# Kernel optimization log

Measured on AMD Instinct MI355X. Metric: run time of the kernel, lower is better.

Reference implementation:

```python
import jax, jax.numpy as jnp
import numpy as np

N_NODES = 100000
N_EDGES = 1600000
F_IN = 128      # dataset.num_features
HID = 128       # hidden_dim (heads=1)
HID_POST = 128  # hidden_dim_post
EDGE_DIM = 16
N_CLASSES = 16
NEG_SLOPE = 0.2  # PyG GATConv default leaky_relu slope


def setup_inputs() -> dict:
    key = jax.random.key(0)
    ks = jax.random.split(key, 16)
    s = 0.1  # weight scale
    inp = {
        "x": jax.random.normal(ks[0], (N_NODES, F_IN), jnp.float32),
        "edge_attr": jax.random.normal(ks[1], (N_EDGES, EDGE_DIM), jnp.float32),
        "W0": jax.random.normal(ks[2], (F_IN, HID), jnp.float32) * s,
        "a_src0": jax.random.normal(ks[3], (HID,), jnp.float32) * s,
        "a_dst0": jax.random.normal(ks[4], (HID,), jnp.float32) * s,
        "We0": jax.random.normal(ks[5], (EDGE_DIM, HID), jnp.float32) * s,
        "a_e0": jax.random.normal(ks[6], (HID,), jnp.float32) * s,
        "b0": jnp.zeros((HID,), jnp.float32),
        "W1": jax.random.normal(ks[7], (HID, HID), jnp.float32) * s,
        "a_src1": jax.random.normal(ks[8], (HID,), jnp.float32) * s,
        "a_dst1": jax.random.normal(ks[9], (HID,), jnp.float32) * s,
        "We1": jax.random.normal(ks[10], (EDGE_DIM, HID), jnp.float32) * s,
        "a_e1": jax.random.normal(ks[11], (HID,), jnp.float32) * s,
        "b1": jnp.zeros((HID,), jnp.float32),
        "lin1_w": jax.random.normal(ks[12], (HID, HID_POST), jnp.float32) * s,
        "lin1_b": jnp.zeros((HID_POST,), jnp.float32),
        "lin2_w": jax.random.normal(ks[13], (HID_POST, N_CLASSES), jnp.float32) * s,
        "lin2_b": jnp.zeros((N_CLASSES,), jnp.float32),
        "edge_index": jax.random.randint(ks[14], (2, N_EDGES), 0, N_NODES, jnp.int64),
    }
    return inp


def gat_conv(x, src, dst, edge_attr, W, a_s, a_d, We, a_e, b):
    """PyG GATConv, heads=1, edge_dim set, add_self_loops=True (fill_value='mean')."""
    n = x.shape[0]
    xl = x @ W                       # [N, HID] shared lin for src/dst
    alpha_src_n = xl @ a_s           # [N]
    alpha_dst_n = xl @ a_d           # [N]
    # self loops: edge_attr filled with per-target-node mean of incoming edge_attr
    deg = jax.ops.segment_sum(jnp.ones(src.shape[0], x.dtype), dst, num_segments=n)
    ea_mean = jax.ops.segment_sum(edge_attr, dst, num_segments=n) / jnp.maximum(deg, 1.0)[:, None]
    loop = jnp.arange(n, dtype=src.dtype)
    src_f = jnp.concatenate([src, loop])
    dst_f = jnp.concatenate([dst, loop])
    ea_f = jnp.concatenate([edge_attr, ea_mean], axis=0)  # [E+N, EDGE_DIM]
    alpha_edge = (ea_f @ We) @ a_e                        # [E+N]
    alpha = jax.nn.leaky_relu(
        alpha_src_n[src_f] + alpha_dst_n[dst_f] + alpha_edge, NEG_SLOPE
    )
    # segment softmax over destination node (every node has its self loop -> nonempty)
    amax = jax.ops.segment_max(alpha, dst_f, num_segments=n)
    ex = jnp.exp(alpha - amax[dst_f])
    denom = jax.ops.segment_sum(ex, dst_f, num_segments=n)
    w = ex / denom[dst_f]                                 # [E+N]
    out = jax.ops.segment_sum(xl[src_f] * w[:, None], dst_f, num_segments=n)
    return out + b


def reference(x, edge_attr, W0, a_src0, a_dst0, We0, a_e0, b0,
              W1, a_src1, a_dst1, We1, a_e1, b1,
              lin1_w, lin1_b, lin2_w, lin2_b, edge_index):
    src, dst = edge_index[0], edge_index[1]
    # dropout layers are identity in eval mode
    h = jax.nn.relu(gat_conv(x, src, dst, edge_attr, W0, a_src0, a_dst0, We0, a_e0, b0))
    h = jax.nn.relu(gat_conv(h, src, dst, edge_attr, W1, a_src1, a_dst1, We1, a_e1, b1))
    h = jax.nn.relu(h @ lin1_w + lin1_b)
    logits = h @ lin2_w + lin2_b
    return jax.nn.log_softmax(logits, axis=-1)
```

## Files before the change

### kernel.cpp

```cpp
#include <hip/hip_runtime.h>
#include <math.h>

#define N_NODES 100000
#define N_EDGES 1600000
#define NEG 0.2f
#define MAXDEG 128
#define WPB 4

__device__ __forceinline__ float lrelu(float x){ return x > 0.f ? x : NEG*x; }
__device__ __forceinline__ unsigned short f2bf(float f){
  unsigned int u = __float_as_uint(f);
  u += 0x7FFFu + ((u >> 16) & 1u);
  return (unsigned short)(u >> 16);
}
__device__ __forceinline__ unsigned xcc_id(){
  unsigned x;
  asm volatile("s_getreg_b32 %0, hwreg(HW_REG_XCC_ID)" : "=s"(x));
  return x & 7u;
}

__global__ __launch_bounds__(256) void k_deg(const int* __restrict__ dst, const float* __restrict__ eatt,
    const float* __restrict__ We0, const float* __restrict__ ae0,
    const float* __restrict__ We1, const float* __restrict__ ae1,
    int* __restrict__ deg8, int* __restrict__ rank, float2* __restrict__ ae01){
  __shared__ float wea[32];
  int t = threadIdx.x;
  if (t < 32){
    const float* W = (t < 16) ? We0 : We1;
    const float* a = (t < 16) ? ae0 : ae1;
    int r = t & 15;
    float acc = 0.f;
    #pragma unroll
    for (int j=0;j<128;j++) acc += W[r*128+j]*a[j];
    wea[t] = acc;
  }
  __syncthreads();
  unsigned xcc = xcc_id();
  int* mydeg = deg8 + (size_t)xcc * N_NODES;
  int e = blockIdx.x*256 + t;
  if (e >= N_EDGES) return;
  const float4* p = (const float4*)(eatt + (size_t)e*16);
  float4 a0=p[0], a1=p[1], a2=p[2], a3=p[3];
  float f0 = a0.x*wea[0] +a0.y*wea[1] +a0.z*wea[2] +a0.w*wea[3]
           + a1.x*wea[4] +a1.y*wea[5] +a1.z*wea[6] +a1.w*wea[7]
           + a2.x*wea[8] +a2.y*wea[9] +a2.z*wea[10]+a2.w*wea[11]
           + a3.x*wea[12]+a3.y*wea[13]+a3.z*wea[14]+a3.w*wea[15];
  float f1 = a0.x*wea[16]+a0.y*wea[17]+a0.z*wea[18]+a0.w*wea[19]
           + a1.x*wea[20]+a1.y*wea[21]+a1.z*wea[22]+a1.w*wea[23]
           + a2.x*wea[24]+a2.y*wea[25]+a2.z*wea[26]+a2.w*wea[27]
           + a3.x*wea[28]+a3.y*wea[29]+a3.z*wea[30]+a3.w*wea[31];
  int r = atomicAdd(&mydeg[dst[e]], 1);
  rank[e] = r | (int)(xcc << 24);
  ae01[e] = make_float2(f0, f1);
}

__global__ __launch_bounds__(256) void k_scan_a(const int* __restrict__ deg8, int* __restrict__ deg,
    int* __restrict__ incl, int* __restrict__ bsum){
  __shared__ int s[256];
  int t = threadIdx.x; int i = blockIdx.x*256 + t;
  int v = 0;
  if (i < N_NODES){
    #pragma unroll
    for (int x=0;x<8;x++) v += deg8[(size_t)x*N_NODES + i];
    deg[i] = v;
  }
  s[t] = v; __syncthreads();
  for (int off=1; off<256; off<<=1){
    int u = (t>=off)? s[t-off] : 0; __syncthreads();
    s[t] += u; __syncthreads();
  }
  if (i < N_NODES) incl[i] = s[t];
  if (t == 255) bsum[blockIdx.x] = s[t];
}
__global__ __launch_bounds__(512) void k_scan_b(const int* __restrict__ bsum, int* __restrict__ bexcl, int nb){
  __shared__ int s[512];
  int t = threadIdx.x;
  int v = (t<nb)? bsum[t] : 0;
  s[t] = v; __syncthreads();
  for (int off=1; off<512; off<<=1){
    int u = (t>=off)? s[t-off] : 0; __syncthreads();
    s[t] += u; __syncthreads();
  }
  if (t<nb) bexcl[t] = s[t]-v;
}
__global__ __launch_bounds__(256) void k_scan_c(const int* __restrict__ incl, const int* __restrict__ deg,
    const int* __restrict__ bexcl, const int* __restrict__ deg8,
    int* __restrict__ rowptr, int* __restrict__ rowptr8){
  int i = blockIdx.x*256+threadIdx.x;
  if (i < N_NODES){
    int base = incl[i] - deg[i] + bexcl[blockIdx.x];
    rowptr[i] = base;
    int run = base;
    #pragma unroll
    for (int x=0;x<8;x++){
      rowptr8[(size_t)i*8 + x] = run;
      run += deg8[(size_t)x*N_NODES + i];
    }
  }
  if (i == 0) rowptr[N_NODES] = N_EDGES;
}

__global__ __launch_bounds__(256) void k_fillf(const int* __restrict__ src, const int* __restrict__ dst,
     const int* __restrict__ rank, const float2* __restrict__ ae01,
     const int* __restrict__ rowptr8, uint4* __restrict__ csr){
  int e = blockIdx.x*256+threadIdx.x;
  if (e >= N_EDGES) return;
  int d = dst[e];
  unsigned rk = (unsigned)rank[e];
  float2 ae = ae01[e];
  int pos = rowptr8[(size_t)d*8 + (rk >> 24)] + (int)(rk & 0xFFFFFFu);
  csr[pos] = make_uint4((unsigned)src[e], __float_as_uint(ae.x), __float_as_uint(ae.y), 0u);
}

__global__ __launch_bounds__(256) void k_gemm(const float* __restrict__ X, const float* __restrict__ W,
    const float* __restrict__ bias, float* __restrict__ Y, unsigned short* __restrict__ Ybf,
    const float* __restrict__ a_s, const float* __restrict__ a_d,
    float* __restrict__ asrc, float* __restrict__ adst, int M, int relu){
  __shared__ float Xs[16][68];
  __shared__ float Ws[16][128];
  __shared__ float as_s[128], ad_s[128];
  int t = threadIdx.x;
  if (a_s && t < 128){ as_s[t] = a_s[t]; ad_s[t] = a_d[t]; }
  int row0 = blockIdx.x * 64;
  int tc = t & 15, tr = t >> 4;
  int c0 = tc*8, r0 = tr*4;
  int lr = t >> 2, lc = (t & 3) << 2;
  int wk = t >> 4, wc = (t & 15) * 8;
  float acc[4][8];
  #pragma unroll
  for (int i=0;i<4;i++)
    #pragma unroll
    for (int j=0;j<8;j++) acc[i][j]=0.f;
  int gr = row0 + lr;
  for (int k0=0; k0<128; k0+=16){
    float4 xv = make_float4(0.f,0.f,0.f,0.f);
    if (gr < M) xv = *(const float4*)(X + (size_t)gr*128 + k0 + lc);
    float4 wv0 = *(const float4*)(W + (size_t)(k0+wk)*128 + wc);
    float4 wv1 = *(const float4*)(W + (size_t)(k0+wk)*128 + wc + 4);
    __syncthreads();
    Xs[lc+0][lr]=xv.x; Xs[lc+1][lr]=xv.y; Xs[lc+2][lr]=xv.z; Xs[lc+3][lr]=xv.w;
    *(float4*)&Ws[wk][wc]   = wv0;
    *(float4*)&Ws[wk][wc+4] = wv1;
    __syncthreads();
    #pragma unroll
    for (int kk=0;kk<16;kk++){
      float4 a  = *(const float4*)&Xs[kk][r0];
      float4 b0 = *(const float4*)&Ws[kk][c0];
      float4 b1 = *(const float4*)&Ws[kk][c0+4];
      float av[4] = {a.x,a.y,a.z,a.w};
      float bv[8] = {b0.x,b0.y,b0.z,b0.w,b1.x,b1.y,b1.z,b1.w};
      #pragma unroll
      for (int i=0;i<4;i++)
        #pragma unroll
        for (int j=0;j<8;j++) acc[i][j] += av[i]*bv[j];
    }
  }
  #pragma unroll
  for (int i=0;i<4;i++){
    int r = row0 + r0 + i;
    float v[8];
    #pragma unroll
    for (int j=0;j<8;j++){
      float u = acc[i][j] + (bias ? bias[c0+j] : 0.f);
      v[j] = relu ? fmaxf(u, 0.f) : u;
    }
    if (r < M){
      if (Y){
        *(float4*)(Y + (size_t)r*128 + c0)     = make_float4(v[0],v[1],v[2],v[3]);
        *(float4*)(Y + (size_t)r*128 + c0 + 4) = make_float4(v[4],v[5],v[6],v[7]);
      }
      if (Ybf){
        uint4 pk;
        pk.x = (unsigned)f2bf(v[0]) | ((unsigned)f2bf(v[1])<<16);
        pk.y = (unsigned)f2bf(v[2]) | ((unsigned)f2bf(v[3])<<16);
        pk.z = (unsigned)f2bf(v[4]) | ((unsigned)f2bf(v[5])<<16);
        pk.w = (unsigned)f2bf(v[6]) | ((unsigned)f2bf(v[7])<<16);
        *(uint4*)(Ybf + (size_t)r*128 + c0) = pk;
      }
    }
    if (a_s){
      float s=0.f, d=0.f;
      #pragma unroll
      for (int j=0;j<8;j++){ s += v[j]*as_s[c0+j]; d += v[j]*ad_s[c0+j]; }
      #pragma unroll
      for (int off=1; off<16; off<<=1){ s += __shfl_xor(s,off); d += __shfl_xor(d,off); }
      if ((t & 15)==0 && r < M){ asrc[r]=s; adst[r]=d; }
    }
  }
}

__global__ __launch_bounds__(256) void k_agg(const int* __restrict__ rowptr, const uint4* __restrict__ csr,
    const float* __restrict__ asrc, const float* __restrict__ adst,
    const unsigned short* __restrict__ xlbf,
    const float* __restrict__ bias, float* __restrict__ out, int relu, int layer){
  int w = threadIdx.x >> 6;
  int lane = threadIdx.x & 63;
  int n = blockIdx.x * WPB + w;
  __shared__ float2 eb[WPB][MAXDEG];
  const char* xbase = (const char*)xlbf;
  int s0 = rowptr[n], s1 = rowptr[n+1];
  int deg = s1 - s0;
  float adst_n = adst[n];
  float m_edge = -1e30f;
  float sae = 0.f;
  for (int base=0; base<deg; base+=64){
    int i = base + lane;
    float a = -1e30f;
    if (i < deg){
      uint4 p4 = csr[s0 + i];
      int sx = (int)p4.x;
      float ae = __uint_as_float(layer ? p4.z : p4.y);
      float av = lrelu(asrc[sx] + adst_n + ae);
      if (i < MAXDEG) eb[w][i] = make_float2(av, __uint_as_float((unsigned)sx << 8));
      a = av;
      sae += ae;
    }
    for (int off=32; off; off>>=1) a = fmaxf(a, __shfl_xor(a, off));
    m_edge = fmaxf(m_edge, a);
  }
  for (int off=32; off; off>>=1) sae += __shfl_xor(sae, off);
  float aloop_n = sae / fmaxf((float)deg, 1.f);
  float al = lrelu(asrc[n] + adst_n + aloop_n);
  float m = fmaxf(m_edge, al);
  float p = 0.f;
  for (int i=lane; i<deg; i+=64){
    float av;
    if (i < MAXDEG) av = eb[w][i].x;
    else { uint4 p4 = csr[s0+i];
           av = lrelu(asrc[p4.x] + adst_n + __uint_as_float(layer ? p4.z : p4.y)); }
    float ev = __expf(av - m);
    if (i < MAXDEG) eb[w][i].x = ev;
    p += ev;
  }
  for (int off=32; off; off>>=1) p += __shfl_xor(p, off);
  float wl = __expf(al - m);
  float denom = p + wl;
  __syncthreads();
  int g = lane >> 4, cl = lane & 15;
  unsigned clb = (unsigned)(cl << 4);
  float acc[8];
  #pragma unroll
  for (int j=0;j<8;j++) acc[j]=0.f;
  if (g == 0){
    uint4 v = *(const uint4*)(xbase + (((unsigned)n << 8) + clb));
    unsigned int uu[4] = {v.x,v.y,v.z,v.w};
    #pragma unroll
    for (int q=0;q<4;q++){
      acc[2*q]   += wl * __uint_as_float(uu[q] << 16);
      acc[2*q+1] += wl * __uint_as_float(uu[q] & 0xFFFF0000u);
    }
  }
  if (deg <= MAXDEG){
    int dfull = deg & ~7;
    for (int i=0; i<dfull; i+=8){
      float2 e0 = eb[w][i+g];
      float2 e1 = eb[w][i+4+g];
      uint4 v0 = *(const uint4*)(xbase + (__float_as_uint(e0.y) + clb));
      uint4 v1 = *(const uint4*)(xbase + (__float_as_uint(e1.y) + clb));
      unsigned int uu0[4] = {v0.x,v0.y,v0.z,v0.w};
      unsigned int uu1[4] = {v1.x,v1.y,v1.z,v1.w};
      #pragma unroll
      for (int q=0;q<4;q++){
        acc[2*q]   += e0.x * __uint_as_float(uu0[q] << 16);
        acc[2*q+1] += e0.x * __uint_as_float(uu0[q] & 0xFFFF0000u);
      }
      #pragma unroll
      for (int q=0;q<4;q++){
        acc[2*q]   += e1.x * __uint_as_float(uu1[q] << 16);
        acc[2*q+1] += e1.x * __uint_as_float(uu1[q] & 0xFFFF0000u);
      }
    }
    for (int i=dfull; i<deg; i+=4){
      int idx = i + g;
      float we = 0.f; unsigned off = (unsigned)n << 8;
      if (idx < deg){ float2 e = eb[w][idx]; we = e.x; off = __float_as_uint(e.y); }
      uint4 v = *(const uint4*)(xbase + (off + clb));
      unsigned int uu[4] = {v.x,v.y,v.z,v.w};
      #pragma unroll
      for (int q=0;q<4;q++){
        acc[2*q]   += we * __uint_as_float(uu[q] << 16);
        acc[2*q+1] += we * __uint_as_float(uu[q] & 0xFFFF0000u);
      }
    }
  } else {
    for (int i=0; i<deg; i+=8){
      int idx0 = i + g, idx1 = i + 4 + g;
      int sx0 = n, sx1 = n; float we0 = 0.f, we1 = 0.f;
      if (idx0 < deg){
        if (idx0 < MAXDEG){ float2 e = eb[w][idx0]; we0 = e.x; sx0 = (int)(__float_as_uint(e.y) >> 8); }
        else { uint4 p4 = csr[s0+idx0]; sx0 = (int)p4.x;
               we0 = __expf(lrelu(asrc[sx0] + adst_n + __uint_as_float(layer ? p4.z : p4.y)) - m); }
      }
      if (idx1 < deg){
        if (idx1 < MAXDEG){ float2 e = eb[w][idx1]; we1 = e.x; sx1 = (int)(__float_as_uint(e.y) >> 8); }
        else { uint4 p4 = csr[s0+idx1]; sx1 = (int)p4.x;
               we1 = __expf(lrelu(asrc[sx1] + adst_n + __uint_as_float(layer ? p4.z : p4.y)) - m); }
      }
      uint4 v0 = *(const uint4*)(xbase + (((unsigned)sx0 << 8) + clb));
      uint4 v1 = *(const uint4*)(xbase + (((unsigned)sx1 << 8) + clb));
      unsigned int uu0[4] = {v0.x,v0.y,v0.z,v0.w};
      unsigned int uu1[4] = {v1.x,v1.y,v1.z,v1.w};
      #pragma unroll
      for (int q=0;q<4;q++){
        acc[2*q]   += we0 * __uint_as_float(uu0[q] << 16);
        acc[2*q+1] += we0 * __uint_as_float(uu0[q] & 0xFFFF0000u);
      }
      #pragma unroll
      for (int q=0;q<4;q++){
        acc[2*q]   += we1 * __uint_as_float(uu1[q] << 16);
        acc[2*q+1] += we1 * __uint_as_float(uu1[q] & 0xFFFF0000u);
      }
    }
  }
  #pragma unroll
  for (int j=0;j<8;j++){
    acc[j] += __shfl_xor(acc[j], 16);
    acc[j] += __shfl_xor(acc[j], 32);
  }
  if (lane < 16){
    float inv = 1.f/denom;
    float4 b0 = *(const float4*)(bias + cl*8);
    float4 b1 = *(const float4*)(bias + cl*8 + 4);
    float o[8];
    o[0]=acc[0]*inv+b0.x; o[1]=acc[1]*inv+b0.y; o[2]=acc[2]*inv+b0.z; o[3]=acc[3]*inv+b0.w;
    o[4]=acc[4]*inv+b1.x; o[5]=acc[5]*inv+b1.y; o[6]=acc[6]*inv+b1.z; o[7]=acc[7]*inv+b1.w;
    if (relu){
      #pragma unroll
      for (int j=0;j<8;j++) o[j]=fmaxf(o[j],0.f);
    }
    *(float4*)(out + (size_t)n*128 + cl*8)     = make_float4(o[0],o[1],o[2],o[3]);
    *(float4*)(out + (size_t)n*128 + cl*8 + 4) = make_float4(o[4],o[5],o[6],o[7]);
  }
}

__global__ __launch_bounds__(256) void k_mlp(const float* __restrict__ X, const float* __restrict__ W,
    const float* __restrict__ bias, const float* __restrict__ w2, const float* __restrict__ b2,
    float* __restrict__ out, int M){
  __shared__ float Xs[16][68];
  __shared__ float Ws[16][128];
  __shared__ float b2s[16];
  int t = threadIdx.x;
  int row0 = blockIdx.x * 64;
  int tc = t & 15, tr = t >> 4;
  int c0 = tc*8, r0 = tr*4;
  int lr = t >> 2, lc = (t & 3) << 2;
  int wk = t >> 4, wc = (t & 15) * 8;
  float acc[4][8];
  #pragma unroll
  for (int i=0;i<4;i++)
    #pragma unroll
    for (int j=0;j<8;j++) acc[i][j]=0.f;
  int gr = row0 + lr;
  for (int k0=0; k0<128; k0+=16){
    float4 xv = make_float4(0.f,0.f,0.f,0.f);
    if (gr < M) xv = *(const float4*)(X + (size_t)gr*128 + k0 + lc);
    float4 wv0 = *(const float4*)(W + (size_t)(k0+wk)*128 + wc);
    float4 wv1 = *(const float4*)(W + (size_t)(k0+wk)*128 + wc + 4);
    __syncthreads();
    Xs[lc+0][lr]=xv.x; Xs[lc+1][lr]=xv.y; Xs[lc+2][lr]=xv.z; Xs[lc+3][lr]=xv.w;
    *(float4*)&Ws[wk][wc]   = wv0;
    *(float4*)&Ws[wk][wc+4] = wv1;
    __syncthreads();
    #pragma unroll
    for (int kk=0;kk<16;kk++){
      float4 a  = *(const float4*)&Xs[kk][r0];
      float4 b0 = *(const float4*)&Ws[kk][c0];
      float4 b1 = *(const float4*)&Ws[kk][c0+4];
      float av[4] = {a.x,a.y,a.z,a.w};
      float bv[8] = {b0.x,b0.y,b0.z,b0.w,b1.x,b1.y,b1.z,b1.w};
      #pragma unroll
      for (int i=0;i<4;i++)
        #pragma unroll
        for (int j=0;j<8;j++) acc[i][j] += av[i]*bv[j];
    }
  }
  __syncthreads();
  float* wflat = &Ws[0][0];
  #pragma unroll
  for (int i=0;i<2;i++) ((float4*)wflat)[t + i*256] = ((const float4*)w2)[t + i*256];
  if (t < 16) b2s[t] = b2[t];
  float4 bba = *(const float4*)(bias + c0);
  float4 bbb = *(const float4*)(bias + c0 + 4);
  float bb[8] = {bba.x,bba.y,bba.z,bba.w,bbb.x,bbb.y,bbb.z,bbb.w};
  #pragma unroll
  for (int i=0;i<4;i++)
    #pragma unroll
    for (int j=0;j<8;j++) acc[i][j] = fmaxf(acc[i][j] + bb[j], 0.f);
  __syncthreads();
  float A0=0.f, A1=0.f, A2=0.f, A3=0.f;
  int sl = (tc+1) & 15;
  #pragma unroll 4
  for (int s=0; s<16; s++){
    int cls = (tc + s) & 15;
    const float* wp = wflat + (size_t)c0*16 + cls;
    float p0=0.f,p1=0.f,p2=0.f,p3=0.f;
    #pragma unroll
    for (int j=0;j<8;j++){
      float wv = wp[j*16];
      p0 += acc[0][j]*wv; p1 += acc[1][j]*wv; p2 += acc[2][j]*wv; p3 += acc[3][j]*wv;
    }
    A0+=p0; A1+=p1; A2+=p2; A3+=p3;
    A0=__shfl(A0,sl,16); A1=__shfl(A1,sl,16); A2=__shfl(A2,sl,16); A3=__shfl(A3,sl,16);
  }
  float A[4] = {A0,A1,A2,A3};
  float bcls = b2s[tc];
  #pragma unroll
  for (int i=0;i<4;i++){
    float v = A[i] + bcls;
    float m = v;
    #pragma unroll
    for (int off=1; off<16; off<<=1) m = fmaxf(m, __shfl_xor(m, off, 16));
    float ex = __expf(v - m);
    float sum = ex;
    #pragma unroll
    for (int off=1; off<16; off<<=1) sum += __shfl_xor(sum, off, 16);
    float lse = m + __logf(sum);
    int r = row0 + r0 + i;
    if (r < M) out[(size_t)r*16 + tc] = v - lse;
  }
}

extern "C" void kernel_launch(void* const* d_in, const int* in_sizes, int n_in,
                              void* d_out, int out_size, void* d_ws, size_t ws_size,
                              hipStream_t stream){
  const float* x    = (const float*)d_in[0];
  const float* eatt = (const float*)d_in[1];
  const float* W0   = (const float*)d_in[2];
  const float* as0  = (const float*)d_in[3];
  const float* ad0  = (const float*)d_in[4];
  const float* We0  = (const float*)d_in[5];
  const float* ae0  = (const float*)d_in[6];
  const float* b0   = (const float*)d_in[7];
  const float* W1   = (const float*)d_in[8];
  const float* as1  = (const float*)d_in[9];
  const float* ad1  = (const float*)d_in[10];
  const float* We1  = (const float*)d_in[11];
  const float* ae1  = (const float*)d_in[12];
  const float* b1   = (const float*)d_in[13];
  const float* l1w  = (const float*)d_in[14];
  const float* l1b  = (const float*)d_in[15];
  const float* l2w  = (const float*)d_in[16];
  const float* l2b  = (const float*)d_in[17];
  const int*   ei   = (const int*)d_in[18];
  const int* srcI = ei;
  const int* dstI = ei + N_EDGES;
  float* out = (float*)d_out;

  char* p = (char*)d_ws;
  auto alloc = [&](size_t bytes)->char*{ char* r = p; p += (bytes + 255) & ~255ull; return r; };
  unsigned short* Abf = (unsigned short*)alloc((size_t)N_NODES*128*2);
  float* B       = (float*)alloc((size_t)N_NODES*128*4);
  float* asrc    = (float*)alloc((size_t)N_NODES*4);
  float* adst    = (float*)alloc((size_t)N_NODES*4);
  int* deg     = (int*)alloc((size_t)N_NODES*4);
  int* rowptr  = (int*)alloc((size_t)(N_NODES+1)*4);
  uint4* csr   = (uint4*)alloc((size_t)N_EDGES*16);
  int* incl    = (int*)alloc((size_t)N_NODES*4);
  int* bsum    = (int*)alloc(512*4);
  int* bexcl   = (int*)alloc(512*4);
  float2* ae01   = (float2*)Abf;
  char*   Bc     = (char*)B;
  int*    rank   = (int*)Bc;
  int*    deg8   = (int*)(Bc + 6400000);
  int*    rowptr8= (int*)(Bc + 6400000 + 3200000);

  const int NB_E = (N_EDGES+255)/256;
  const int NB_N = (N_NODES+255)/256;
  const int NB_W = N_NODES/WPB;
  const int NB_G = (N_NODES+63)/64;

  hipMemsetAsync(deg8, 0, (size_t)8*N_NODES*4, stream);
  k_deg   <<<NB_E,256,0,stream>>>(dstI, eatt, We0, ae0, We1, ae1, deg8, rank, ae01);
  k_scan_a<<<NB_N,256,0,stream>>>(deg8, deg, incl, bsum);
  k_scan_b<<<1,  512,0,stream>>>(bsum, bexcl, NB_N);
  k_scan_c<<<NB_N,256,0,stream>>>(incl, deg, bexcl, deg8, rowptr, rowptr8);
  k_fillf <<<NB_E,256,0,stream>>>(srcI, dstI, rank, ae01, rowptr8, csr);

  k_gemm <<<NB_G,256,0,stream>>>(x, W0, nullptr, nullptr, Abf, as0, ad0, asrc, adst, N_NODES, 0);
  k_agg  <<<NB_W,256,0,stream>>>(rowptr, csr, asrc, adst, Abf, b0, B, 1, 0);

  k_gemm <<<NB_G,256,0,stream>>>(B, W1, nullptr, nullptr, Abf, as1, ad1, asrc, adst, N_NODES, 0);
  k_agg  <<<NB_W,256,0,stream>>>(rowptr, csr, asrc, adst, Abf, b1, B, 1, 1);

  k_mlp  <<<NB_G,256,0,stream>>>(B, l1w, l1b, l2w, l2b, out, N_NODES);
}
```

Measured before the change: 636.6 us.

## Fuse edge preprocessing with layer-0 GEMM and use a single global degree counter

```diff
diff --git a/kernel.cpp b/kernel.cpp
--- a/kernel.cpp
+++ b/kernel.cpp
@@ -13,57 +13,110 @@
   u += 0x7FFFu + ((u >> 16) & 1u);
   return (unsigned short)(u >> 16);
 }
-__device__ __forceinline__ unsigned xcc_id(){
-  unsigned x;
-  asm volatile("s_getreg_b32 %0, hwreg(HW_REG_XCC_ID)" : "=s"(x));
-  return x & 7u;
-}
-
-__global__ __launch_bounds__(256) void k_deg(const int* __restrict__ dst, const float* __restrict__ eatt,
+
+__global__ __launch_bounds__(256) void k_pre(const int* __restrict__ dst, const float* __restrict__ eatt,
     const float* __restrict__ We0, const float* __restrict__ ae0,
     const float* __restrict__ We1, const float* __restrict__ ae1,
-    int* __restrict__ deg8, int* __restrict__ rank, float2* __restrict__ ae01){
-  __shared__ float wea[32];
+    int* __restrict__ deg, int* __restrict__ rank, float2* __restrict__ ae01,
+    const float* __restrict__ X, const float* __restrict__ W,
+    const float* __restrict__ a_s, const float* __restrict__ a_d,
+    unsigned short* __restrict__ Ybf, float* __restrict__ asrc, float* __restrict__ adst){
+  __shared__ float Xs[16][68];
+  __shared__ float Ws[16][128];
+  __shared__ float as_s[128], ad_s[128];
   int t = threadIdx.x;
-  if (t < 32){
-    const float* W = (t < 16) ? We0 : We1;
-    const float* a = (t < 16) ? ae0 : ae1;
-    int r = t & 15;
-    float acc = 0.f;
-    #pragma unroll
-    for (int j=0;j<128;j++) acc += W[r*128+j]*a[j];
-    wea[t] = acc;
-  }
-  __syncthreads();
-  unsigned xcc = xcc_id();
-  int* mydeg = deg8 + (size_t)xcc * N_NODES;
-  int e = blockIdx.x*256 + t;
-  if (e >= N_EDGES) return;
-  const float4* p = (const float4*)(eatt + (size_t)e*16);
-  float4 a0=p[0], a1=p[1], a2=p[2], a3=p[3];
-  float f0 = a0.x*wea[0] +a0.y*wea[1] +a0.z*wea[2] +a0.w*wea[3]
-           + a1.x*wea[4] +a1.y*wea[5] +a1.z*wea[6] +a1.w*wea[7]
-           + a2.x*wea[8] +a2.y*wea[9] +a2.z*wea[10]+a2.w*wea[11]
-           + a3.x*wea[12]+a3.y*wea[13]+a3.z*wea[14]+a3.w*wea[15];
-  float f1 = a0.x*wea[16]+a0.y*wea[17]+a0.z*wea[18]+a0.w*wea[19]
-           + a1.x*wea[20]+a1.y*wea[21]+a1.z*wea[22]+a1.w*wea[23]
-           + a2.x*wea[24]+a2.y*wea[25]+a2.z*wea[26]+a2.w*wea[27]
-           + a3.x*wea[28]+a3.y*wea[29]+a3.z*wea[30]+a3.w*wea[31];
-  int r = atomicAdd(&mydeg[dst[e]], 1);
-  rank[e] = r | (int)(xcc << 24);
-  ae01[e] = make_float2(f0, f1);
-}
-
-__global__ __launch_bounds__(256) void k_scan_a(const int* __restrict__ deg8, int* __restrict__ deg,
-    int* __restrict__ incl, int* __restrict__ bsum){
+  int bid = blockIdx.x;
+  int rem = bid % 5;
+  if (rem != 4){
+    float* wea = &Ws[0][0];
+    if (t < 32){
+      const float* Wm = (t < 16) ? We0 : We1;
+      const float* am = (t < 16) ? ae0 : ae1;
+      int r = t & 15;
+      float acc = 0.f;
+      #pragma unroll
+      for (int j=0;j<128;j++) acc += Wm[r*128+j]*am[j];
+      wea[t] = acc;
+    }
+    __syncthreads();
+    int e = ((bid/5)*4 + rem)*256 + t;
+    if (e >= N_EDGES) return;
+    const float4* p = (const float4*)(eatt + (size_t)e*16);
+    float4 a0=p[0], a1=p[1], a2=p[2], a3=p[3];
+    float f0 = a0.x*wea[0] +a0.y*wea[1] +a0.z*wea[2] +a0.w*wea[3]
+             + a1.x*wea[4] +a1.y*wea[5] +a1.z*wea[6] +a1.w*wea[7]
+             + a2.x*wea[8] +a2.y*wea[9] +a2.z*wea[10]+a2.w*wea[11]
+             + a3.x*wea[12]+a3.y*wea[13]+a3.z*wea[14]+a3.w*wea[15];
+    float f1 = a0.x*wea[16]+a0.y*wea[17]+a0.z*wea[18]+a0.w*wea[19]
+             + a1.x*wea[20]+a1.y*wea[21]+a1.z*wea[22]+a1.w*wea[23]
+             + a2.x*wea[24]+a2.y*wea[25]+a2.z*wea[26]+a2.w*wea[27]
+             + a3.x*wea[28]+a3.y*wea[29]+a3.z*wea[30]+a3.w*wea[31];
+    rank[e] = atomicAdd(&deg[dst[e]], 1);
+    ae01[e] = make_float2(f0, f1);
+    return;
+  }
+  if (t < 128){ as_s[t] = a_s[t]; ad_s[t] = a_d[t]; }
+  int row0 = (bid/5) * 64;
+  int tc = t & 15, tr = t >> 4;
+  int c0 = tc*8, r0 = tr*4;
+  int lr = t >> 2, lc = (t & 3) << 2;
+  int wk = t >> 4, wc = (t & 15) * 8;
+  float acc[4][8];
+  #pragma unroll
+  for (int i=0;i<4;i++)
+    #pragma unroll
+    for (int j=0;j<8;j++) acc[i][j]=0.f;
+  int gr = row0 + lr;
+  for (int k0=0; k0<128; k0+=16){
+    float4 xv = make_float4(0.f,0.f,0.f,0.f);
+    if (gr < N_NODES) xv = *(const float4*)(X + (size_t)gr*128 + k0 + lc);
+    float4 wv0 = *(const float4*)(W + (size_t)(k0+wk)*128 + wc);
+    float4 wv1 = *(const float4*)(W + (size_t)(k0+wk)*128 + wc + 4);
+    __syncthreads();
+    Xs[lc+0][lr]=xv.x; Xs[lc+1][lr]=xv.y; Xs[lc+2][lr]=xv.z; Xs[lc+3][lr]=xv.w;
+    *(float4*)&Ws[wk][wc]   = wv0;
+    *(float4*)&Ws[wk][wc+4] = wv1;
+    __syncthreads();
+    #pragma unroll
+    for (int kk=0;kk<16;kk++){
+      float4 a  = *(const float4*)&Xs[kk][r0];
+      float4 b0 = *(const float4*)&Ws[kk][c0];
+      float4 b1 = *(const float4*)&Ws[kk][c0+4];
+      float av[4] = {a.x,a.y,a.z,a.w};
+      float bv[8] = {b0.x,b0.y,b0.z,b0.w,b1.x,b1.y,b1.z,b1.w};
+      #pragma unroll
+      for (int i=0;i<4;i++)
+        #pragma unroll
+        for (int j=0;j<8;j++) acc[i][j] += av[i]*bv[j];
+    }
+  }
+  #pragma unroll
+  for (int i=0;i<4;i++){
+    int r = row0 + r0 + i;
+    float v[8];
+    #pragma unroll
+    for (int j=0;j<8;j++) v[j] = acc[i][j];
+    if (r < N_NODES){
+      uint4 pk;
+      pk.x = (unsigned)f2bf(v[0]) | ((unsigned)f2bf(v[1])<<16);
+      pk.y = (unsigned)f2bf(v[2]) | ((unsigned)f2bf(v[3])<<16);
+      pk.z = (unsigned)f2bf(v[4]) | ((unsigned)f2bf(v[5])<<16);
+      pk.w = (unsigned)f2bf(v[6]) | ((unsigned)f2bf(v[7])<<16);
+      *(uint4*)(Ybf + (size_t)r*128 + c0) = pk;
+    }
+    float s=0.f, d=0.f;
+    #pragma unroll
+    for (int j=0;j<8;j++){ s += v[j]*as_s[c0+j]; d += v[j]*ad_s[c0+j]; }
+    #pragma unroll
+    for (int off=1; off<16; off<<=1){ s += __shfl_xor(s,off); d += __shfl_xor(d,off); }
+    if ((t & 15)==0 && r < N_NODES){ asrc[r]=s; adst[r]=d; }
+  }
+}
+
+__global__ __launch_bounds__(256) void k_scan_a(const int* __restrict__ deg, int* __restrict__ incl, int* __restrict__ bsum){
   __shared__ int s[256];
   int t = threadIdx.x; int i = blockIdx.x*256 + t;
-  int v = 0;
-  if (i < N_NODES){
-    #pragma unroll
-    for (int x=0;x<8;x++) v += deg8[(size_t)x*N_NODES + i];
-    deg[i] = v;
-  }
+  int v = (i < N_NODES) ? deg[i] : 0;
   s[t] = v; __syncthreads();
   for (int off=1; off<256; off<<=1){
     int u = (t>=off)? s[t-off] : 0; __syncthreads();
@@ -84,31 +137,20 @@
   if (t<nb) bexcl[t] = s[t]-v;
 }
 __global__ __launch_bounds__(256) void k_scan_c(const int* __restrict__ incl, const int* __restrict__ deg,
-    const int* __restrict__ bexcl, const int* __restrict__ deg8,
-    int* __restrict__ rowptr, int* __restrict__ rowptr8){
+    const int* __restrict__ bexcl, int* __restrict__ rowptr){
   int i = blockIdx.x*256+threadIdx.x;
-  if (i < N_NODES){
-    int base = incl[i] - deg[i] + bexcl[blockIdx.x];
-    rowptr[i] = base;
-    int run = base;
-    #pragma unroll
-    for (int x=0;x<8;x++){
-      rowptr8[(size_t)i*8 + x] = run;
-      run += deg8[(size_t)x*N_NODES + i];
-    }
-  }
+  if (i < N_NODES) rowptr[i] = incl[i] - deg[i] + bexcl[blockIdx.x];
   if (i == 0) rowptr[N_NODES] = N_EDGES;
 }
 
 __global__ __launch_bounds__(256) void k_fillf(const int* __restrict__ src, const int* __restrict__ dst,
      const int* __restrict__ rank, const float2* __restrict__ ae01,
-     const int* __restrict__ rowptr8, uint4* __restrict__ csr){
+     const int* __restrict__ rowptr, uint4* __restrict__ csr){
   int e = blockIdx.x*256+threadIdx.x;
   if (e >= N_EDGES) return;
   int d = dst[e];
-  unsigned rk = (unsigned)rank[e];
   float2 ae = ae01[e];
-  int pos = rowptr8[(size_t)d*8 + (rk >> 24)] + (int)(rk & 0xFFFFFFu);
+  int pos = rowptr[d] + rank[e];
   csr[pos] = make_uint4((unsigned)src[e], __float_as_uint(ae.x), __float_as_uint(ae.y), 0u);
 }
 
@@ -458,25 +500,24 @@
   int* incl    = (int*)alloc((size_t)N_NODES*4);
   int* bsum    = (int*)alloc(512*4);
   int* bexcl   = (int*)alloc(512*4);
-  float2* ae01   = (float2*)Abf;
-  char*   Bc     = (char*)B;
-  int*    rank   = (int*)Bc;
-  int*    deg8   = (int*)(Bc + 6400000);
-  int*    rowptr8= (int*)(Bc + 6400000 + 3200000);
+  char*   Bc   = (char*)B;
+  int*    rank = (int*)Bc;
+  float2* ae01 = (float2*)(Bc + 6400000);
 
   const int NB_E = (N_EDGES+255)/256;
   const int NB_N = (N_NODES+255)/256;
   const int NB_W = N_NODES/WPB;
   const int NB_G = (N_NODES+63)/64;
-
-  hipMemsetAsync(deg8, 0, (size_t)8*N_NODES*4, stream);
-  k_deg   <<<NB_E,256,0,stream>>>(dstI, eatt, We0, ae0, We1, ae1, deg8, rank, ae01);
-  k_scan_a<<<NB_N,256,0,stream>>>(deg8, deg, incl, bsum);
+  const int NB_P = 7815;
+
+  hipMemsetAsync(deg, 0, (size_t)N_NODES*4, stream);
+  k_pre  <<<NB_P,256,0,stream>>>(dstI, eatt, We0, ae0, We1, ae1, deg, rank, ae01,
+                                 x, W0, as0, ad0, Abf, asrc, adst);
+  k_scan_a<<<NB_N,256,0,stream>>>(deg, incl, bsum);
   k_scan_b<<<1,  512,0,stream>>>(bsum, bexcl, NB_N);
-  k_scan_c<<<NB_N,256,0,stream>>>(incl, deg, bexcl, deg8, rowptr, rowptr8);
-  k_fillf <<<NB_E,256,0,stream>>>(srcI, dstI, rank, ae01, rowptr8, csr);
-
-  k_gemm <<<NB_G,256,0,stream>>>(x, W0, nullptr, nullptr, Abf, as0, ad0, asrc, adst, N_NODES, 0);
+  k_scan_c<<<NB_N,256,0,stream>>>(incl, deg, bexcl, rowptr);
+  k_fillf <<<NB_E,256,0,stream>>>(srcI, dstI, rank, ae01, rowptr, csr);
+
   k_agg  <<<NB_W,256,0,stream>>>(rowptr, csr, asrc, adst, Abf, b0, B, 1, 0);
 
   k_gemm <<<NB_G,256,0,stream>>>(B, W1, nullptr, nullptr, Abf, as1, ad1, asrc, adst, N_NODES, 0);
```

After: 602.1 us. 1.06x faster.

## Build CSR via two-level bucket partition instead of global-atomic counting sort

Applied to the files above, without the earlier changes.

```diff
diff --git a/kernel.cpp b/kernel.cpp
--- a/kernel.cpp
+++ b/kernel.cpp
@@ -6,6 +6,8 @@
 #define NEG 0.2f
 #define MAXDEG 128
 #define WPB 4
+#define NBK 391
+#define CHK 6250
 
 __device__ __forceinline__ float lrelu(float x){ return x > 0.f ? x : NEG*x; }
 __device__ __forceinline__ unsigned short f2bf(float f){
@@ -13,103 +15,129 @@
   u += 0x7FFFu + ((u >> 16) & 1u);
   return (unsigned short)(u >> 16);
 }
-__device__ __forceinline__ unsigned xcc_id(){
-  unsigned x;
-  asm volatile("s_getreg_b32 %0, hwreg(HW_REG_XCC_ID)" : "=s"(x));
-  return x & 7u;
-}
-
-__global__ __launch_bounds__(256) void k_deg(const int* __restrict__ dst, const float* __restrict__ eatt,
+
+
+__global__ __launch_bounds__(512) void k_count(const int* __restrict__ dst, int* __restrict__ gcount){
+  __shared__ unsigned hist[NBK];
+  int t = threadIdx.x;
+  for (int b=t; b<NBK; b+=512) hist[b]=0;
+  __syncthreads();
+  int base = blockIdx.x * CHK;
+  for (int i=t; i<CHK; i+=512){
+    int d = dst[base+i];
+    atomicAdd(&hist[d>>8], 1u);
+  }
+  __syncthreads();
+  for (int b=t; b<NBK; b+=512){
+    unsigned h = hist[b];
+    if (h) atomicAdd(&gcount[b], (int)h);
+  }
+}
+
+__global__ __launch_bounds__(512) void k_bscan(const int* __restrict__ gcount,
+    int* __restrict__ gbase, int* __restrict__ gcursor,
     const float* __restrict__ We0, const float* __restrict__ ae0,
     const float* __restrict__ We1, const float* __restrict__ ae1,
-    int* __restrict__ deg8, int* __restrict__ rank, float2* __restrict__ ae01){
+    float* __restrict__ wea01, int* __restrict__ rowptr){
+  __shared__ int s[512];
+  int t = threadIdx.x;
+  int v = (t<NBK)? gcount[t] : 0;
+  s[t]=v; __syncthreads();
+  for (int off=1; off<512; off<<=1){
+    int u = (t>=off)? s[t-off]:0; __syncthreads();
+    s[t]+=u; __syncthreads();
+  }
+  if (t<NBK){ int e = s[t]-v; gbase[t]=e; gcursor[t]=e; }
+  if (t==NBK) gbase[NBK]=N_EDGES;
+  if (t==0) rowptr[N_NODES]=N_EDGES;
+  if (t<32){
+    const float* W = (t<16)? We0 : We1;
+    const float* a = (t<16)? ae0 : ae1;
+    int r = t & 15;
+    float acc = 0.f;
+    #pragma unroll
+    for (int j=0;j<128;j++) acc += W[r*128+j]*a[j];
+    wea01[t]=acc;
+  }
+}
+
+__global__ __launch_bounds__(512) void k_part(const int* __restrict__ dst,
+    int* __restrict__ gcursor, unsigned* __restrict__ part){
+  __shared__ unsigned hist[NBK];
+  __shared__ int bbase[NBK];
+  __shared__ unsigned cur[NBK];
+  int t = threadIdx.x;
+  for (int b=t; b<NBK; b+=512) hist[b]=0;
+  __syncthreads();
+  int base = blockIdx.x * CHK;
+  for (int i=t; i<CHK; i+=512) atomicAdd(&hist[dst[base+i]>>8], 1u);
+  __syncthreads();
+  for (int b=t; b<NBK; b+=512){
+    unsigned h = hist[b];
+    bbase[b] = h ? atomicAdd(&gcursor[b], (int)h) : 0;
+    cur[b]=0;
+  }
+  __syncthreads();
+  for (int i=t; i<CHK; i+=512){
+    int e = base+i;
+    int d = dst[e];
+    int bin = d>>8;
+    unsigned off = atomicAdd(&cur[bin], 1u);
+    part[bbase[bin]+(int)off] = (unsigned)e | ((unsigned)(d&255)<<21);
+  }
+}
+
+__global__ __launch_bounds__(512) void k_build(const int* __restrict__ gbase,
+    const unsigned* __restrict__ part, const int* __restrict__ src,
+    const float* __restrict__ eatt, const float* __restrict__ wea01,
+    int* __restrict__ rowptr, uint4* __restrict__ csr){
+  __shared__ unsigned cnt[256];
+  __shared__ int rb[256];
+  __shared__ unsigned s[256];
   __shared__ float wea[32];
   int t = threadIdx.x;
-  if (t < 32){
-    const float* W = (t < 16) ? We0 : We1;
-    const float* a = (t < 16) ? ae0 : ae1;
-    int r = t & 15;
-    float acc = 0.f;
-    #pragma unroll
-    for (int j=0;j<128;j++) acc += W[r*128+j]*a[j];
-    wea[t] = acc;
-  }
-  __syncthreads();
-  unsigned xcc = xcc_id();
-  int* mydeg = deg8 + (size_t)xcc * N_NODES;
-  int e = blockIdx.x*256 + t;
-  if (e >= N_EDGES) return;
-  const float4* p = (const float4*)(eatt + (size_t)e*16);
-  float4 a0=p[0], a1=p[1], a2=p[2], a3=p[3];
-  float f0 = a0.x*wea[0] +a0.y*wea[1] +a0.z*wea[2] +a0.w*wea[3]
-           + a1.x*wea[4] +a1.y*wea[5] +a1.z*wea[6] +a1.w*wea[7]
-           + a2.x*wea[8] +a2.y*wea[9] +a2.z*wea[10]+a2.w*wea[11]
-           + a3.x*wea[12]+a3.y*wea[13]+a3.z*wea[14]+a3.w*wea[15];
-  float f1 = a0.x*wea[16]+a0.y*wea[17]+a0.z*wea[18]+a0.w*wea[19]
-           + a1.x*wea[20]+a1.y*wea[21]+a1.z*wea[22]+a1.w*wea[23]
-           + a2.x*wea[24]+a2.y*wea[25]+a2.z*wea[26]+a2.w*wea[27]
-           + a3.x*wea[28]+a3.y*wea[29]+a3.z*wea[30]+a3.w*wea[31];
-  int r = atomicAdd(&mydeg[dst[e]], 1);
-  rank[e] = r | (int)(xcc << 24);
-  ae01[e] = make_float2(f0, f1);
-}
-
-__global__ __launch_bounds__(256) void k_scan_a(const int* __restrict__ deg8, int* __restrict__ deg,
-    int* __restrict__ incl, int* __restrict__ bsum){
-  __shared__ int s[256];
-  int t = threadIdx.x; int i = blockIdx.x*256 + t;
-  int v = 0;
-  if (i < N_NODES){
-    #pragma unroll
-    for (int x=0;x<8;x++) v += deg8[(size_t)x*N_NODES + i];
-    deg[i] = v;
-  }
-  s[t] = v; __syncthreads();
+  int b = blockIdx.x;
+  int lo = gbase[b], hi = gbase[b+1];
+  if (t<32) wea[t]=wea01[t];
+  if (t<256) cnt[t]=0;
+  __syncthreads();
+  for (int i=lo+t; i<hi; i+=512) atomicAdd(&cnt[part[i]>>21], 1u);
+  __syncthreads();
+  if (t<256) s[t]=cnt[t];
+  __syncthreads();
   for (int off=1; off<256; off<<=1){
-    int u = (t>=off)? s[t-off] : 0; __syncthreads();
-    s[t] += u; __syncthreads();
-  }
-  if (i < N_NODES) incl[i] = s[t];
-  if (t == 255) bsum[blockIdx.x] = s[t];
-}
-__global__ __launch_bounds__(512) void k_scan_b(const int* __restrict__ bsum, int* __restrict__ bexcl, int nb){
-  __shared__ int s[512];
-  int t = threadIdx.x;
-  int v = (t<nb)? bsum[t] : 0;
-  s[t] = v; __syncthreads();
-  for (int off=1; off<512; off<<=1){
-    int u = (t>=off)? s[t-off] : 0; __syncthreads();
-    s[t] += u; __syncthreads();
-  }
-  if (t<nb) bexcl[t] = s[t]-v;
-}
-__global__ __launch_bounds__(256) void k_scan_c(const int* __restrict__ incl, const int* __restrict__ deg,
-    const int* __restrict__ bexcl, const int* __restrict__ deg8,
-    int* __restrict__ rowptr, int* __restrict__ rowptr8){
-  int i = blockIdx.x*256+threadIdx.x;
-  if (i < N_NODES){
-    int base = incl[i] - deg[i] + bexcl[blockIdx.x];
-    rowptr[i] = base;
-    int run = base;
-    #pragma unroll
-    for (int x=0;x<8;x++){
-      rowptr8[(size_t)i*8 + x] = run;
-      run += deg8[(size_t)x*N_NODES + i];
-    }
-  }
-  if (i == 0) rowptr[N_NODES] = N_EDGES;
-}
-
-__global__ __launch_bounds__(256) void k_fillf(const int* __restrict__ src, const int* __restrict__ dst,
-     const int* __restrict__ rank, const float2* __restrict__ ae01,
-     const int* __restrict__ rowptr8, uint4* __restrict__ csr){
-  int e = blockIdx.x*256+threadIdx.x;
-  if (e >= N_EDGES) return;
-  int d = dst[e];
-  unsigned rk = (unsigned)rank[e];
-  float2 ae = ae01[e];
-  int pos = rowptr8[(size_t)d*8 + (rk >> 24)] + (int)(rk & 0xFFFFFFu);
-  csr[pos] = make_uint4((unsigned)src[e], __float_as_uint(ae.x), __float_as_uint(ae.y), 0u);
+    unsigned u = 0;
+    if (t<256 && t>=off) u = s[t-off];
+    __syncthreads();
+    if (t<256) s[t]+=u;
+    __syncthreads();
+  }
+  if (t<256){
+    int bn = lo + (int)(s[t]-cnt[t]);
+    rb[t]=bn;
+    int node = (b<<8)+t;
+    if (node < N_NODES) rowptr[node]=bn;
+    cnt[t]=0;
+  }
+  __syncthreads();
+  for (int i=lo+t; i<hi; i+=512){
+    unsigned p = part[i];
+    int eid = (int)(p & 0x1FFFFFu);
+    int dl  = (int)(p >> 21);
+    const float4* pe = (const float4*)(eatt + (size_t)eid*16);
+    float4 a0=pe[0], a1=pe[1], a2=pe[2], a3=pe[3];
+    float f0 = a0.x*wea[0] +a0.y*wea[1] +a0.z*wea[2] +a0.w*wea[3]
+             + a1.x*wea[4] +a1.y*wea[5] +a1.z*wea[6] +a1.w*wea[7]
+             + a2.x*wea[8] +a2.y*wea[9] +a2.z*wea[10]+a2.w*wea[11]
+             + a3.x*wea[12]+a3.y*wea[13]+a3.z*wea[14]+a3.w*wea[15];
+    float f1 = a0.x*wea[16]+a0.y*wea[17]+a0.z*wea[18]+a0.w*wea[19]
+             + a1.x*wea[20]+a1.y*wea[21]+a1.z*wea[22]+a1.w*wea[23]
+             + a2.x*wea[24]+a2.y*wea[25]+a2.z*wea[26]+a2.w*wea[27]
+             + a3.x*wea[28]+a3.y*wea[29]+a3.z*wea[30]+a3.w*wea[31];
+    int sx = src[eid];
+    unsigned off = atomicAdd(&cnt[dl], 1u);
+    csr[rb[dl]+(int)off] = make_uint4((unsigned)sx, __float_as_uint(f0), __float_as_uint(f1), 0u);
+  }
 }
 
 __global__ __launch_bounds__(256) void k_gemm(const float* __restrict__ X, const float* __restrict__ W,
@@ -452,31 +480,24 @@
   float* B       = (float*)alloc((size_t)N_NODES*128*4);
   float* asrc    = (float*)alloc((size_t)N_NODES*4);
   float* adst    = (float*)alloc((size_t)N_NODES*4);
-  int* deg     = (int*)alloc((size_t)N_NODES*4);
   int* rowptr  = (int*)alloc((size_t)(N_NODES+1)*4);
   uint4* csr   = (uint4*)alloc((size_t)N_EDGES*16);
-  int* incl    = (int*)alloc((size_t)N_NODES*4);
-  int* bsum    = (int*)alloc(512*4);
-  int* bexcl   = (int*)alloc(512*4);
-  float2* ae01   = (float2*)Abf;
-  char*   Bc     = (char*)B;
-  int*    rank   = (int*)Bc;
-  int*    deg8   = (int*)(Bc + 6400000);
-  int*    rowptr8= (int*)(Bc + 6400000 + 3200000);
-
-  const int NB_E = (N_EDGES+255)/256;
-  const int NB_N = (N_NODES+255)/256;
+  int* gcount  = (int*)alloc(400*4);
+  int* gbase   = (int*)alloc(400*4);
+  int* gcursor = (int*)alloc(400*4);
+  float* wea01 = (float*)alloc(128);
+  unsigned* part = (unsigned*)B;
+
   const int NB_W = N_NODES/WPB;
   const int NB_G = (N_NODES+63)/64;
 
-  hipMemsetAsync(deg8, 0, (size_t)8*N_NODES*4, stream);
-  k_deg   <<<NB_E,256,0,stream>>>(dstI, eatt, We0, ae0, We1, ae1, deg8, rank, ae01);
-  k_scan_a<<<NB_N,256,0,stream>>>(deg8, deg, incl, bsum);
-  k_scan_b<<<1,  512,0,stream>>>(bsum, bexcl, NB_N);
-  k_scan_c<<<NB_N,256,0,stream>>>(incl, deg, bexcl, deg8, rowptr, rowptr8);
-  k_fillf <<<NB_E,256,0,stream>>>(srcI, dstI, rank, ae01, rowptr8, csr);
-
+  hipMemsetAsync(gcount, 0, 400*4, stream);
+  k_count<<<256,512,0,stream>>>(dstI, gcount);
+  k_bscan<<<1,  512,0,stream>>>(gcount, gbase, gcursor, We0, ae0, We1, ae1, wea01, rowptr);
+  k_part <<<256,512,0,stream>>>(dstI, gcursor, part);
   k_gemm <<<NB_G,256,0,stream>>>(x, W0, nullptr, nullptr, Abf, as0, ad0, asrc, adst, N_NODES, 0);
+  k_build<<<NBK,512,0,stream>>>(gbase, part, srcI, eatt, wea01, rowptr, csr);
+
   k_agg  <<<NB_W,256,0,stream>>>(rowptr, csr, asrc, adst, Abf, b0, B, 1, 0);
 
   k_gemm <<<NB_G,256,0,stream>>>(B, W1, nullptr, nullptr, Abf, as1, ad1, asrc, adst, N_NODES, 0);
```

New measurement: 634.4 us. Within noise of the previous version (-0.3%).
